# Performance work log

Measured on AMD Instinct MI355X. Metric: run time of the kernel, lower is better.

The kernel has to match this reference:

```python
import jax, jax.numpy as jnp
import numpy as np

# dims
B, T, C, D, H, NH, HD, INTER, L = 4, 1024, 256, 256, 512, 8, 64, 2048, 4
CF, CB, BASE = 0, 128, 10000.0  # context_forward, context_backward, rope theta


def _rope_tables():
    inv = 1.0 / (BASE ** (jnp.arange(0, HD, 2, dtype=jnp.float32) / HD))
    t = jnp.arange(T, dtype=jnp.float32)
    f = jnp.einsum('i,j->ij', t, inv)          # [T, HD/2]
    emb = jnp.concatenate([f, f], axis=-1)      # [T, HD]
    return jnp.cos(emb), jnp.sin(emb)


def _rotate_half(x):
    x1, x2 = jnp.split(x, 2, axis=-1)
    return jnp.concatenate([-x2, x1], axis=-1)


def _ln(x, g, b):
    m = x.mean(-1, keepdims=True)
    v = ((x - m) ** 2).mean(-1, keepdims=True)
    return (x - m) / jnp.sqrt(v + 1e-5) * g + b


def _band_mask():
    # create_context_mask(CF, CB, T): allow j in [i-CB, i+CF]
    i = jnp.arange(T)[:, None]
    j = jnp.arange(T)[None, :]
    return (j <= i + CF) & (j >= i - CB)  # [T, T] bool


def setup_inputs() -> dict:
    key = jax.random.key(0)
    ks = jax.random.split(key, 16)
    w = lambda k, shp: (0.02 * jax.random.normal(k, shp)).astype(jnp.float32)
    return {
        'spikes': jax.random.normal(ks[0], (B, T, C), dtype=jnp.float32),
        'spikes_mask': jnp.ones((B, T), dtype=jnp.int32),
        'spikes_timestamp': jnp.tile(jnp.arange(T, dtype=jnp.int32), (B, 1)),
        'embed_w': w(ks[1], (C, D)), 'embed_b': jnp.zeros((D,), jnp.float32),
        'proj_w': w(ks[2], (D, H)), 'proj_b': jnp.zeros((H,), jnp.float32),
        'ln1_g': jnp.ones((L, H), jnp.float32), 'ln1_b': jnp.zeros((L, H), jnp.float32),
        'Wq': w(ks[3], (L, H, H)), 'bq': jnp.zeros((L, H), jnp.float32),
        'Wk': w(ks[4], (L, H, H)), 'bk': jnp.zeros((L, H), jnp.float32),
        'Wv': w(ks[5], (L, H, H)), 'bv': jnp.zeros((L, H), jnp.float32),
        'Wo': w(ks[6], (L, H, H)), 'bo': jnp.zeros((L, H), jnp.float32),
        'ln2_g': jnp.ones((L, H), jnp.float32), 'ln2_b': jnp.zeros((L, H), jnp.float32),
        'up_w': w(ks[7], (L, H, INTER)), 'up_b': jnp.zeros((L, INTER), jnp.float32),
        'down_w': w(ks[8], (L, INTER, H)), 'down_b': jnp.zeros((L, H), jnp.float32),
    }


def reference(spikes, spikes_mask, spikes_timestamp, embed_w, embed_b, proj_w, proj_b,
              ln1_g, ln1_b, Wq, bq, Wk, bk, Wv, bv, Wo, bo, ln2_g, ln2_b,
              up_w, up_b, down_w, down_b):
    cos, sin = _rope_tables()
    mask = _band_mask()[None, None] & (spikes_mask[:, None, None, :] > 0)  # [B,1,T,T]
    cs = cos[spikes_timestamp][:, None]  # [B,1,T,HD]
    sn = sin[spikes_timestamp][:, None]
    neg = jnp.finfo(jnp.float32).min

    # NeuralEmbeddingLayer (no stack/pos/tokens): Linear -> gelu -> Linear
    x = jax.nn.gelu(spikes @ embed_w + embed_b, approximate=False) @ proj_w + proj_b

    for l in range(L):
        h = _ln(x, ln1_g[l], ln1_b[l])
        q = (h @ Wq[l] + bq[l]).reshape(B, T, NH, HD).transpose(0, 2, 1, 3)
        k = (h @ Wk[l] + bk[l]).reshape(B, T, NH, HD).transpose(0, 2, 1, 3)
        v = (h @ Wv[l] + bv[l]).reshape(B, T, NH, HD).transpose(0, 2, 1, 3)
        q = q * cs + _rotate_half(q) * sn
        k = k * cs + _rotate_half(k) * sn
        s = jnp.einsum('bhqd,bhkd->bhqk', q, k) / np.float32(np.sqrt(HD))
        s = jnp.where(mask, s, neg)
        p = jax.nn.softmax(s, axis=-1)
        o = jnp.einsum('bhqk,bhkd->bhqd', p, v).transpose(0, 2, 1, 3).reshape(B, T, H)
        x = x + o @ Wo[l] + bo[l]
        h = _ln(x, ln2_g[l], ln2_b[l])
        x = x + jax.nn.gelu(h @ up_w[l] + up_b[l], approximate=False) @ down_w[l] + down_b[l]
    return x
```

## Files before the change

### kernel.cpp

```cpp
#include <hip/hip_runtime.h>
#include <math.h>

#define B_ 4
#define T_ 1024
#define C_ 256
#define D_ 256
#define H_ 512
#define NH_ 8
#define HD_ 64
#define INTER_ 2048
#define L_ 4
#define CB_ 128

typedef short bf16x8 __attribute__((ext_vector_type(8)));
typedef unsigned short ush8 __attribute__((ext_vector_type(8)));
typedef float f32x4 __attribute__((ext_vector_type(4)));

__device__ __forceinline__ float gelu_exact(float x) {
    return 0.5f * x * (1.0f + erff(x * 0.70710678118654752f));
}

__device__ __forceinline__ unsigned short f2bf(float f) {
    unsigned u = __float_as_uint(f);
    u += 0x7fffu + ((u >> 16) & 1u);
    return (unsigned short)(u >> 16);
}
__device__ __forceinline__ float bf2f(unsigned short h) {
    return __uint_as_float((unsigned)h << 16);
}

__device__ __forceinline__ void xcd_swz(int& bx, int& by) {
    const int gx  = gridDim.x;
    const int nwg = gx * gridDim.y;
    int bid = blockIdx.y * gx + blockIdx.x;
    bid = (bid & 7) * (nwg >> 3) + (bid >> 3);
    bx = bid % gx;
    by = bid / gx;
}

template<int ACT, int RES, int OBF, int SPLIT>
__global__ __launch_bounds__(256) void mm64_k(
    const unsigned short* __restrict__ A, const unsigned short* __restrict__ BT,
    const float* __restrict__ b0, const float* __restrict__ b1,
    const float* __restrict__ b2,
    const float* res,
    void* o0, void* o1, void* o2,
    const int M, const int N, const int K)
{
    __shared__ unsigned short As[64 * 256];
    __shared__ unsigned short Bs[64 * 256];

    int bx, by; xcd_swz(bx, by);

    const int tid  = threadIdx.x;
    const int lane = tid & 63;
    const int w    = tid >> 6;
    const int m0   = by * 64;
    const int n0   = bx * 64;
    const int wm   = (w >> 1) * 32;
    const int wn   = (w & 1) * 32;
    const int l16  = lane & 15;
    const int g16  = lane >> 4;

    f32x4 acc[2][2] = {};

    const unsigned short* Abase = A  + (size_t)m0 * K;
    const unsigned short* Bbase = BT + (size_t)n0 * K;

    for (int k0 = 0; k0 < K; k0 += 256) {
        __syncthreads();
#pragma unroll
        for (int it = 0; it < 8; ++it) {
            const int c  = it * 256 + tid;
            const int rc = c >> 5;
            const int gk = (c & 31) ^ (rc & 7);
            __builtin_amdgcn_global_load_lds(
                (const __attribute__((address_space(1))) unsigned*)(Abase + (size_t)rc * K + k0 + gk * 8),
                (__attribute__((address_space(3))) unsigned*)(As + (size_t)(it * 256 + (w << 6)) * 8), 16, 0, 0);
        }
#pragma unroll
        for (int it = 0; it < 8; ++it) {
            const int c  = it * 256 + tid;
            const int rc = c >> 5;
            const int gk = (c & 31) ^ (rc & 7);
            __builtin_amdgcn_global_load_lds(
                (const __attribute__((address_space(1))) unsigned*)(Bbase + (size_t)rc * K + k0 + gk * 8),
                (__attribute__((address_space(3))) unsigned*)(Bs + (size_t)(it * 256 + (w << 6)) * 8), 16, 0, 0);
        }
        __syncthreads();

#pragma unroll
        for (int kk = 0; kk < 8; ++kk) {
            const int kf = kk * 4 + g16;
            const int sw = (kf ^ (l16 & 7)) * 8;
            bf16x8 a[2], b[2];
#pragma unroll
            for (int t = 0; t < 2; ++t)
                a[t] = *(const bf16x8*)&As[(wm + t * 16 + l16) * 256 + sw];
#pragma unroll
            for (int t = 0; t < 2; ++t)
                b[t] = *(const bf16x8*)&Bs[(wn + t * 16 + l16) * 256 + sw];
#pragma unroll
            for (int i = 0; i < 2; ++i)
#pragma unroll
                for (int j = 0; j < 2; ++j)
                    acc[i][j] = __builtin_amdgcn_mfma_f32_16x16x32_bf16(a[i], b[j], acc[i][j], 0, 0, 0);
        }
    }

    if (OBF || SPLIT) {
        __syncthreads();
        unsigned short* Eb = ((w < 2) ? As : Bs) + (w & 1) * 1024;
        const int row16 = lane >> 2;
        const int cg    = lane & 3;

        const int gnb   = n0 + wn;
        const int which = SPLIT ? (gnb >> 9) : 0;
        const int lnb   = SPLIT ? (gnb & 511) : gnb;
        const int ldo   = SPLIT ? 512 : N;
        unsigned short* oo = SPLIT
            ? ((which == 0) ? (unsigned short*)o0 : (which == 1) ? (unsigned short*)o1 : (unsigned short*)o2)
            : (unsigned short*)o0;
        const float* bb = SPLIT ? ((which == 0) ? b0 : (which == 1) ? b1 : b2) : b0;
        const float scale = (SPLIT && which == 0) ? 0.125f : 1.0f;

#pragma unroll
        for (int i = 0; i < 2; ++i) {
#pragma unroll
            for (int j = 0; j < 2; ++j) {
                const float bv = bb[lnb + j * 16 + l16];
#pragma unroll
                for (int r = 0; r < 4; ++r) {
                    float cv = acc[i][j][r] + bv;
                    if (ACT) cv = gelu_exact(cv);
                    if (SPLIT) cv *= scale;
                    Eb[(g16 * 4 + r) * 40 + j * 16 + l16] = f2bf(cv);
                }
            }
            const int grow0 = m0 + wm + i * 16 + row16;
#pragma unroll
            for (int s = 0; s < 2; ++s) {
                ushort4 t4 = *(const ushort4*)&Eb[row16 * 40 + s * 16 + cg * 4];
                *(ushort4*)&oo[(size_t)grow0 * ldo + lnb + s * 16 + cg * 4] = t4;
            }
        }
        return;
    }

#pragma unroll
    for (int i = 0; i < 2; ++i) {
        const int gmb = m0 + wm + i * 16 + g16 * 4;
#pragma unroll
        for (int j = 0; j < 2; ++j) {
            const int gn = n0 + wn + j * 16 + l16;
            const float bv = b0[gn];
#pragma unroll
            for (int r = 0; r < 4; ++r) {
                float cv = acc[i][j][r] + bv;
                if (ACT) cv = gelu_exact(cv);
                if (RES) cv += res[(size_t)(gmb + r) * 512 + gn];
                ((float*)o0)[(size_t)(gmb + r) * N + gn] = cv;
            }
        }
    }
}

template<int ACT, int RES, int OBF, int SPLIT, int BN>
__global__ __launch_bounds__(256) void mm128_k(
    const unsigned short* __restrict__ A, const unsigned short* __restrict__ BT,
    const float* __restrict__ b0, const float* __restrict__ b1,
    const float* __restrict__ b2,
    const float* res,
    void* o0, void* o1, void* o2,
    const int M, const int N, const int K)
{
    constexpr int NJ = BN / 32;

    __shared__ unsigned short As[128 * 128];
    __shared__ unsigned short Bs[BN * 128];

    int bx, by; xcd_swz(bx, by);

    const int tid  = threadIdx.x;
    const int lane = tid & 63;
    const int w    = tid >> 6;
    const int m0   = by * 128;
    const int n0   = bx * BN;
    const int wm   = (w >> 1) * 64;
    const int wn   = (w & 1) * (BN / 2);
    const int l16  = lane & 15;
    const int g16  = lane >> 4;

    f32x4 acc[4][NJ] = {};

    const unsigned short* Abase = A  + (size_t)m0 * K;
    const unsigned short* Bbase = BT + (size_t)n0 * K;

    for (int k0 = 0; k0 < K; k0 += 128) {
        __syncthreads();
#pragma unroll
        for (int it = 0; it < 8; ++it) {
            const int c  = it * 256 + tid;
            const int rc = c >> 4;
            const int gk = (c & 15) ^ (rc & 7);
            __builtin_amdgcn_global_load_lds(
                (const __attribute__((address_space(1))) unsigned*)(Abase + (size_t)rc * K + k0 + gk * 8),
                (__attribute__((address_space(3))) unsigned*)(As + (size_t)(it * 256 + (w << 6)) * 8), 16, 0, 0);
        }
#pragma unroll
        for (int it = 0; it < NJ * 2; ++it) {
            const int c  = it * 256 + tid;
            const int rc = c >> 4;
            const int gk = (c & 15) ^ (rc & 7);
            __builtin_amdgcn_global_load_lds(
                (const __attribute__((address_space(1))) unsigned*)(Bbase + (size_t)rc * K + k0 + gk * 8),
                (__attribute__((address_space(3))) unsigned*)(Bs + (size_t)(it * 256 + (w << 6)) * 8), 16, 0, 0);
        }
        __syncthreads();

#pragma unroll
        for (int kk = 0; kk < 4; ++kk) {
            const int kf = kk * 4 + g16;
            const int sw = (kf ^ (l16 & 7)) * 8;
            bf16x8 a[4], b[NJ];
#pragma unroll
            for (int t = 0; t < 4; ++t)
                a[t] = *(const bf16x8*)&As[(wm + t * 16 + l16) * 128 + sw];
#pragma unroll
            for (int t = 0; t < NJ; ++t)
                b[t] = *(const bf16x8*)&Bs[(wn + t * 16 + l16) * 128 + sw];
#pragma unroll
            for (int i = 0; i < 4; ++i)
#pragma unroll
                for (int j = 0; j < NJ; ++j)
                    acc[i][j] = __builtin_amdgcn_mfma_f32_16x16x32_bf16(a[i], b[j], acc[i][j], 0, 0, 0);
        }
    }

    if (OBF || SPLIT) {
        __syncthreads();
        constexpr int WC  = NJ * 16;
        constexpr int EST = WC + 8;
        constexpr int LPR = WC / 4;
        constexpr int RPI = 64 / LPR;
        unsigned short* Eb = As + w * (16 * EST);
        const int erow = lane / LPR;
        const int ecol = (lane % LPR) * 4;

        const int gnb   = n0 + wn;
        const int which = SPLIT ? (gnb >> 9) : 0;
        const int lnb   = SPLIT ? (gnb & 511) : gnb;
        const int ldo   = SPLIT ? 512 : N;
        unsigned short* oo = SPLIT
            ? ((which == 0) ? (unsigned short*)o0 : (which == 1) ? (unsigned short*)o1 : (unsigned short*)o2)
            : (unsigned short*)o0;
        const float* bb = SPLIT ? ((which == 0) ? b0 : (which == 1) ? b1 : b2) : b0;
        const float scale = (SPLIT && which == 0) ? 0.125f : 1.0f;

#pragma unroll
        for (int i = 0; i < 4; ++i) {
#pragma unroll
            for (int j = 0; j < NJ; ++j) {
                const float bv = bb[lnb + j * 16 + l16];
#pragma unroll
                for (int r = 0; r < 4; ++r) {
                    float cv = acc[i][j][r] + bv;
                    if (ACT) cv = gelu_exact(cv);
                    if (SPLIT) cv *= scale;
                    Eb[(g16 * 4 + r) * EST + j * 16 + l16] = f2bf(cv);
                }
            }
            const int grow0 = m0 + wm + i * 16;
#pragma unroll
            for (int s = 0; s < NJ; ++s) {
                ushort4 t4 = *(const ushort4*)&Eb[(s * RPI + erow) * EST + ecol];
                *(ushort4*)&oo[(size_t)(grow0 + s * RPI + erow) * ldo + lnb + ecol] = t4;
            }
        }
        return;
    }

#pragma unroll
    for (int i = 0; i < 4; ++i) {
        const int gmb = m0 + wm + i * 16 + g16 * 4;
#pragma unroll
        for (int j = 0; j < NJ; ++j) {
            const int gn = n0 + wn + j * 16 + l16;
            const float bv = b0[gn];
#pragma unroll
            for (int r = 0; r < 4; ++r) {
                float cv = acc[i][j][r] + bv;
                if (ACT) cv = gelu_exact(cv);
                if (RES) cv += res[(size_t)(gmb + r) * 512 + gn];
                ((float*)o0)[(size_t)(gmb + r) * N + gn] = cv;
            }
        }
    }
}

__global__ __launch_bounds__(256) void prep_k(
    const float* __restrict__ spikes,
    const float* __restrict__ embed_w, const float* __restrict__ proj_w,
    const float* __restrict__ Wq, const float* __restrict__ Wk,
    const float* __restrict__ Wv, const float* __restrict__ Wo,
    const float* __restrict__ up_w, const float* __restrict__ down_w,
    unsigned short* __restrict__ spbf,
    unsigned short* __restrict__ embT, unsigned short* __restrict__ projT,
    unsigned short* __restrict__ qkvT, unsigned short* __restrict__ woT,
    unsigned short* __restrict__ upT, unsigned short* __restrict__ downT)
{
    const int idx = blockIdx.x;
    const int tid = threadIdx.x;

    if (idx >= 3120) {
        const int base = (idx - 3120) * 4096 + tid * 16;
#pragma unroll
        for (int s = 0; s < 4; ++s) {
            float4 v = *(const float4*)&spikes[base + s * 4];
            ushort4 o = {f2bf(v.x), f2bf(v.y), f2bf(v.z), f2bf(v.w)};
            *(ushort4*)&spbf[base + s * 4] = o;
        }
        return;
    }

    const float* src; unsigned short* dst; int R, Cc, t;
    if (idx < 16)      { src = embed_w; dst = embT;  R = C_; Cc = D_; t = idx; }
    else if (idx < 48) { src = proj_w;  dst = projT; R = D_; Cc = H_; t = idx - 16; }
    else if (idx < 816) {
        const int j = idx - 48;
        const int wsel = j >> 8;
        const int l = (j & 255) >> 6;
        t = j & 63;
        src = ((wsel == 0) ? Wq : (wsel == 1) ? Wk : Wv) + (size_t)l * H_ * H_;
        dst = qkvT + (size_t)l * 3 * H_ * H_ + (size_t)wsel * H_ * H_;
        R = H_; Cc = H_;
    } else if (idx < 1072) {
        const int j = idx - 816; const int l = j >> 6; t = j & 63;
        src = Wo + (size_t)l * H_ * H_; dst = woT + (size_t)l * H_ * H_;
        R = H_; Cc = H_;
    } else if (idx < 2096) {
        const int j = idx - 1072; const int l = j >> 8; t = j & 255;
        src = up_w + (size_t)l * H_ * INTER_; dst = upT + (size_t)l * INTER_ * H_;
        R = H_; Cc = INTER_;
    } else {
        const int j = idx - 2096; const int l = j >> 8; t = j & 255;
        src = down_w + (size_t)l * INTER_ * H_; dst = downT + (size_t)l * H_ * INTER_;
        R = INTER_; Cc = H_;
    }
    const int ntx = Cc >> 6;
    const int c0 = (t % ntx) * 64, r0 = (t / ntx) * 64;

    __shared__ float tile[64][65];
    const int tr = tid >> 4, tc = (tid & 15) * 4;
#pragma unroll
    for (int i = 0; i < 4; ++i) {
        float4 v = *(const float4*)&src[(size_t)(r0 + tr + i * 16) * Cc + c0 + tc];
        tile[tr + i * 16][tc + 0] = v.x;
        tile[tr + i * 16][tc + 1] = v.y;
        tile[tr + i * 16][tc + 2] = v.z;
        tile[tr + i * 16][tc + 3] = v.w;
    }
    __syncthreads();
#pragma unroll
    for (int i = 0; i < 4; ++i) {
        const int n = tr + i * 16;
        ushort4 o;
        o.x = f2bf(tile[tc + 0][n]);
        o.y = f2bf(tile[tc + 1][n]);
        o.z = f2bf(tile[tc + 2][n]);
        o.w = f2bf(tile[tc + 3][n]);
        *(ushort4*)&dst[(size_t)(c0 + n) * R + r0 + tc] = o;
    }
}

__global__ __launch_bounds__(256) void ln_k(
    const float* __restrict__ x, const float* __restrict__ g,
    const float* __restrict__ b, unsigned short* __restrict__ out)
{
    const int row = blockIdx.x;
    const int tid = threadIdx.x;
    const float* xr = x + (size_t)row * H_;

    float v0 = xr[tid];
    float v1 = xr[tid + 256];

    float s = v0 + v1;
#pragma unroll
    for (int off = 32; off; off >>= 1) s += __shfl_xor(s, off);

    __shared__ float red[4];
    const int wave = tid >> 6;
    if ((tid & 63) == 0) red[wave] = s;
    __syncthreads();
    const float mean = (red[0] + red[1] + red[2] + red[3]) * (1.0f / (float)H_);

    const float d0 = v0 - mean, d1 = v1 - mean;
    float q = d0 * d0 + d1 * d1;
#pragma unroll
    for (int off = 32; off; off >>= 1) q += __shfl_xor(q, off);
    __syncthreads();
    if ((tid & 63) == 0) red[wave] = q;
    __syncthreads();
    const float var = (red[0] + red[1] + red[2] + red[3]) * (1.0f / (float)H_);
    const float rstd = rsqrtf(var + 1e-5f);

    out[(size_t)row * H_ + tid]       = f2bf(d0 * rstd * g[tid] + b[tid]);
    out[(size_t)row * H_ + tid + 256] = f2bf(d1 * rstd * g[tid + 256] + b[tid + 256]);
}

#define AWIN 192
#define AKS 72
#define AVS 200

__global__ __launch_bounds__(256) void attn_k(
    const unsigned short* __restrict__ q, const unsigned short* __restrict__ k,
    const unsigned short* __restrict__ v, const int* __restrict__ smask,
    const int* __restrict__ ts, unsigned short* __restrict__ o)
{
    __shared__ unsigned short Ks[AWIN * AKS];
    __shared__ unsigned short Vt[64 * AVS];
    unsigned short* const Pb = Ks;

    const int blk = blockIdx.x;
    const int qt = blk & 15;
    const int h  = (blk >> 4) & 7;
    const int b  = blk >> 7;
    const int tid  = threadIdx.x;
    const int lane = tid & 63;
    const int w    = tid >> 6;
    const int l16  = lane & 15;
    const int g16  = lane >> 4;

    const int qlo = qt * 64;
    const int klo = (qlo >= CB_) ? (qlo - CB_) : 0;
    const int tb  = b * 1024;

    bf16x8 qa0, qa1;
    {
        const int qrow = w * 16 + l16;
        const unsigned short* gq = q + ((size_t)(tb + qlo + qrow)) * 512 + h * 64;
        ush8 lo = *(const ush8*)&gq[g16 * 8];
        ush8 hi = *(const ush8*)&gq[g16 * 8 + 32];
        const float tstamp = (float)ts[tb + qlo + qrow];
#pragma unroll
        for (int j = 0; j < 8; ++j) {
            const int d = g16 * 8 + j;
            const float freq = __expf(-0.2878231366242558f * (float)d);
            const float ang = tstamp * freq;
            const float cc = __cosf(ang), ss = __sinf(ang);
            const float v1 = bf2f(lo[j]);
            const float v2 = bf2f(hi[j]);
            ((unsigned short*)&qa0)[j] = f2bf(v1 * cc - v2 * ss);
            ((unsigned short*)&qa1)[j] = f2bf(v2 * cc + v1 * ss);
        }
    }

    {
        const unsigned short* gk = k + ((size_t)(tb + klo)) * 512 + h * 64;
        for (int c = tid; c < AWIN * 8; c += 256) {
            const int row = c >> 3, c4 = (c & 7) * 4;
            ushort4 lo = *(const ushort4*)&gk[(size_t)row * 512 + c4];
            ushort4 hi = *(const ushort4*)&gk[(size_t)row * 512 + c4 + 32];
            const float tstamp = (float)ts[tb + klo + row];
            ushort4 olo, ohi;
#pragma unroll
            for (int j2 = 0; j2 < 4; ++j2) {
                const float freq = __expf(-0.2878231366242558f * (float)(c4 + j2));
                const float ang = tstamp * freq;
                const float cc = __cosf(ang), ss = __sinf(ang);
                const float v1 = bf2f(((const unsigned short*)&lo)[j2]);
                const float v2 = bf2f(((const unsigned short*)&hi)[j2]);
                ((unsigned short*)&olo)[j2] = f2bf(v1 * cc - v2 * ss);
                ((unsigned short*)&ohi)[j2] = f2bf(v2 * cc + v1 * ss);
            }
            *(ushort4*)&Ks[row * AKS + c4]      = olo;
            *(ushort4*)&Ks[row * AKS + c4 + 32] = ohi;
        }
    }
    {
        const unsigned short* gv = v + ((size_t)(tb + klo)) * 512 + h * 64;
        for (int c = tid; c < AWIN * 16; c += 256) {
            const int row = c >> 4, c4 = (c & 15) * 4;
            ushort4 vv = *(const ushort4*)&gv[(size_t)row * 512 + c4];
            Vt[(c4 + 0) * AVS + row] = vv.x;
            Vt[(c4 + 1) * AVS + row] = vv.y;
            Vt[(c4 + 2) * AVS + row] = vv.z;
            Vt[(c4 + 3) * AVS + row] = vv.w;
        }
    }
    __syncthreads();

    f32x4 accs[12];
#pragma unroll
    for (int t = 0; t < 12; ++t) {
        const bf16x8 b0 = *(const bf16x8*)&Ks[(t * 16 + l16) * AKS + g16 * 8];
        const bf16x8 b1 = *(const bf16x8*)&Ks[(t * 16 + l16) * AKS + 32 + g16 * 8];
        f32x4 c = {};
        c = __builtin_amdgcn_mfma_f32_16x16x32_bf16(qa0, b0, c, 0, 0, 0);
        c = __builtin_amdgcn_mfma_f32_16x16x32_bf16(qa1, b1, c, 0, 0, 0);
        accs[t] = c;
    }

    bool mk[12];
    int  jj[12];
#pragma unroll
    for (int t = 0; t < 12; ++t) {
        jj[t] = klo + t * 16 + l16;
        mk[t] = smask[tb + jj[t]] > 0;
    }

    float rs[4];
#pragma unroll
    for (int r = 0; r < 4; ++r) {
        const int i = qlo + 16 * w + g16 * 4 + r;
        float mx = -1e30f;
#pragma unroll
        for (int t = 0; t < 12; ++t) {
            const bool val = mk[t] && (jj[t] >= i - CB_) && (jj[t] <= i);
            mx = fmaxf(mx, val ? accs[t][r] : -1e30f);
        }
        mx = fmaxf(mx, __shfl_xor(mx, 1));
        mx = fmaxf(mx, __shfl_xor(mx, 2));
        mx = fmaxf(mx, __shfl_xor(mx, 4));
        mx = fmaxf(mx, __shfl_xor(mx, 8));
        float sum = 0.0f;
#pragma unroll
        for (int t = 0; t < 12; ++t) {
            const bool val = mk[t] && (jj[t] >= i - CB_) && (jj[t] <= i);
            const float p = val ? __expf(accs[t][r] - mx) : 0.0f;
            accs[t][r] = p;
            sum += p;
        }
        sum += __shfl_xor(sum, 1);
        sum += __shfl_xor(sum, 2);
        sum += __shfl_xor(sum, 4);
        sum += __shfl_xor(sum, 8);
        rs[r] = 1.0f / sum;
    }

    __syncthreads();

#pragma unroll
    for (int t = 0; t < 12; ++t)
#pragma unroll
        for (int r = 0; r < 4; ++r)
            Pb[(16 * w + g16 * 4 + r) * AVS + t * 16 + l16] = f2bf(accs[t][r]);

    f32x4 acco[4];
#pragma unroll
    for (int nt = 0; nt < 4; ++nt) {
        f32x4 c = {};
#pragma unroll
        for (int ks = 0; ks < 6; ++ks) {
            const bf16x8 a = *(const bf16x8*)&Pb[(16 * w + l16) * AVS + ks * 32 + g16 * 8];
            const bf16x8 bb = *(const bf16x8*)&Vt[(nt * 16 + l16) * AVS + ks * 32 + g16 * 8];
            c = __builtin_amdgcn_mfma_f32_16x16x32_bf16(a, bb, c, 0, 0, 0);
        }
        acco[nt] = c;
    }

    __syncthreads();
#pragma unroll
    for (int nt = 0; nt < 4; ++nt)
#pragma unroll
        for (int r = 0; r < 4; ++r)
            Pb[(16 * w + g16 * 4 + r) * AVS + nt * 16 + l16] = f2bf(acco[nt][r] * rs[r]);

    const int row16 = lane >> 2, cg = lane & 3;
    const int grow = tb + qlo + 16 * w + row16;
#pragma unroll
    for (int s = 0; s < 4; ++s) {
        ushort4 t4 = *(const ushort4*)&Pb[(16 * w + row16) * AVS + s * 16 + cg * 4];
        *(ushort4*)&o[(size_t)grow * 512 + h * 64 + s * 16 + cg * 4] = t4;
    }
}

extern "C" void kernel_launch(void* const* d_in, const int* in_sizes, int n_in,
                              void* d_out, int out_size, void* d_ws, size_t ws_size,
                              hipStream_t stream)
{
    const float* spikes  = (const float*)d_in[0];
    const int*   smask   = (const int*)d_in[1];
    const int*   ts      = (const int*)d_in[2];
    const float* embed_w = (const float*)d_in[3];
    const float* embed_b = (const float*)d_in[4];
    const float* proj_w  = (const float*)d_in[5];
    const float* proj_b  = (const float*)d_in[6];
    const float* ln1_g   = (const float*)d_in[7];
    const float* ln1_b   = (const float*)d_in[8];
    const float* Wq      = (const float*)d_in[9];
    const float* bq      = (const float*)d_in[10];
    const float* Wk      = (const float*)d_in[11];
    const float* bk      = (const float*)d_in[12];
    const float* Wv      = (const float*)d_in[13];
    const float* bv      = (const float*)d_in[14];
    const float* Wo      = (const float*)d_in[15];
    const float* bo      = (const float*)d_in[16];
    const float* ln2_g   = (const float*)d_in[17];
    const float* ln2_b   = (const float*)d_in[18];
    const float* up_w    = (const float*)d_in[19];
    const float* up_b    = (const float*)d_in[20];
    const float* down_w  = (const float*)d_in[21];
    const float* down_b  = (const float*)d_in[22];

    const int M = B_ * T_;

    char* p = (char*)d_ws;
    float* x = (float*)p;                       p += (size_t)M * H_ * 4;
    unsigned short* qb  = (unsigned short*)p;   p += (size_t)M * H_ * 2;
    unsigned short* kb  = (unsigned short*)p;   p += (size_t)M * H_ * 2;
    unsigned short* vb  = (unsigned short*)p;   p += (size_t)M * H_ * 2;
    unsigned short* hbf = (unsigned short*)p;   p += (size_t)M * H_ * 2;
    unsigned short* obf = (unsigned short*)p;   p += (size_t)M * H_ * 2;
    unsigned short* ibf = (unsigned short*)p;   p += (size_t)M * INTER_ * 2;
    unsigned short* tbf = (unsigned short*)p;   p += (size_t)M * D_ * 2;
    unsigned short* spbf  = (unsigned short*)p; p += (size_t)M * C_ * 2;
    unsigned short* embT  = (unsigned short*)p; p += (size_t)D_ * C_ * 2;
    unsigned short* projT = (unsigned short*)p; p += (size_t)H_ * D_ * 2;
    unsigned short* qkvT  = (unsigned short*)p; p += (size_t)L_ * 3 * H_ * H_ * 2;
    unsigned short* woT   = (unsigned short*)p; p += (size_t)L_ * H_ * H_ * 2;
    unsigned short* upT   = (unsigned short*)p; p += (size_t)L_ * INTER_ * H_ * 2;
    unsigned short* downT = (unsigned short*)p; p += (size_t)L_ * H_ * INTER_ * 2;

    prep_k<<<3376, 256, 0, stream>>>(
        spikes, embed_w, proj_w, Wq, Wk, Wv, Wo, up_w, down_w,
        spbf, embT, projT, qkvT, woT, upT, downT);

    mm64_k<1, 0, 1, 0><<<dim3(D_ / 64, M / 64), 256, 0, stream>>>(
        spbf, embT, embed_b, nullptr, nullptr, nullptr,
        tbf, nullptr, nullptr, M, D_, C_);
    mm64_k<0, 0, 0, 0><<<dim3(H_ / 64, M / 64), 256, 0, stream>>>(
        tbf, projT, proj_b, nullptr, nullptr, nullptr,
        x, nullptr, nullptr, M, H_, D_);

    for (int l = 0; l < L_; ++l) {
        const unsigned short* qkvT_l = qkvT + (size_t)l * 3 * H_ * H_;
        const unsigned short* woT_l  = woT  + (size_t)l * H_ * H_;
        const unsigned short* upT_l  = upT  + (size_t)l * INTER_ * H_;
        const unsigned short* dnT_l  = downT + (size_t)l * H_ * INTER_;

        ln_k<<<M, 256, 0, stream>>>(x, ln1_g + l * H_, ln1_b + l * H_, hbf);

        mm128_k<0, 0, 1, 1, 64><<<dim3((3 * H_) / 64, M / 128), 256, 0, stream>>>(
            hbf, qkvT_l, bq + l * H_, bk + l * H_, bv + l * H_, nullptr,
            qb, kb, vb, M, 3 * H_, H_);

        attn_k<<<B_ * NH_ * (T_ / 64), 256, 0, stream>>>(qb, kb, vb, smask, ts, obf);

        mm64_k<0, 1, 0, 0><<<dim3(H_ / 64, M / 64), 256, 0, stream>>>(
            obf, woT_l, bo + l * H_, nullptr, nullptr, x,
            x, nullptr, nullptr, M, H_, H_);

        ln_k<<<M, 256, 0, stream>>>(x, ln2_g + l * H_, ln2_b + l * H_, hbf);

        mm128_k<1, 0, 1, 0, 128><<<dim3(INTER_ / 128, M / 128), 256, 0, stream>>>(
            hbf, upT_l, up_b + l * INTER_, nullptr, nullptr, nullptr,
            ibf, nullptr, nullptr, M, INTER_, H_);

        float* dst = (l == L_ - 1) ? (float*)d_out : x;
        mm64_k<0, 1, 0, 0><<<dim3(H_ / 64, M / 64), 256, 0, stream>>>(
            ibf, dnT_l, down_b + l * H_, nullptr, nullptr, x,
            dst, nullptr, nullptr, M, H_, INTER_);
    }
}
```

Baseline: 493.8 us.

## Precompute RoPE cos/sin table once and make LayerNorm one row per wave

Adds a RoPE cos/sin table, computed once per call in extra prep_k blocks from the timestamps, and has the attention kernel read it instead of evaluating exp/cos/sin for every Q and K element in every layer. LayerNorm now gives each row to one wavefront with vectorized float4 loads and shuffle-only reductions, which removes the shared-memory reductions and block barriers and cuts the block count by four. In exchange the table adds global-memory traffic (M*32 float2 values) and the prep kernel launches extra blocks.

```diff
diff --git a/kernel.cpp b/kernel.cpp
--- a/kernel.cpp
+++ b/kernel.cpp
@@ -304,13 +304,29 @@
     const float* __restrict__ Wq, const float* __restrict__ Wk,
     const float* __restrict__ Wv, const float* __restrict__ Wo,
     const float* __restrict__ up_w, const float* __restrict__ down_w,
+    const int* __restrict__ ts,
     unsigned short* __restrict__ spbf,
     unsigned short* __restrict__ embT, unsigned short* __restrict__ projT,
     unsigned short* __restrict__ qkvT, unsigned short* __restrict__ woT,
-    unsigned short* __restrict__ upT, unsigned short* __restrict__ downT)
+    unsigned short* __restrict__ upT, unsigned short* __restrict__ downT,
+    float2* __restrict__ rope_tab)
 {
     const int idx = blockIdx.x;
     const int tid = threadIdx.x;
+
+    if (idx >= 3376) {
+        const int e0 = (idx - 3376) * 4096 + tid * 16;
+#pragma unroll
+        for (int i = 0; i < 16; ++i) {
+            const int e = e0 + i;
+            const int row = e >> 5, d = e & 31;
+            const float tstamp = (float)ts[row];
+            const float freq = __expf(-0.2878231366242558f * (float)d);
+            const float ang = tstamp * freq;
+            rope_tab[e] = make_float2(__cosf(ang), __sinf(ang));
+        }
+        return;
+    }
 
     if (idx >= 3120) {
         const int base = (idx - 3120) * 4096 + tid * 16;
@@ -377,35 +393,46 @@
     const float* __restrict__ x, const float* __restrict__ g,
     const float* __restrict__ b, unsigned short* __restrict__ out)
 {
-    const int row = blockIdx.x;
-    const int tid = threadIdx.x;
+    const int wave = threadIdx.x >> 6;
+    const int lane = threadIdx.x & 63;
+    const int row  = blockIdx.x * 4 + wave;
     const float* xr = x + (size_t)row * H_;
-
-    float v0 = xr[tid];
-    float v1 = xr[tid + 256];
-
-    float s = v0 + v1;
+    const int c0 = lane * 8;
+
+    float4 a0 = *(const float4*)&xr[c0];
+    float4 a1 = *(const float4*)&xr[c0 + 4];
+
+    float s = a0.x + a0.y + a0.z + a0.w + a1.x + a1.y + a1.z + a1.w;
 #pragma unroll
     for (int off = 32; off; off >>= 1) s += __shfl_xor(s, off);
-
-    __shared__ float red[4];
-    const int wave = tid >> 6;
-    if ((tid & 63) == 0) red[wave] = s;
-    __syncthreads();
-    const float mean = (red[0] + red[1] + red[2] + red[3]) * (1.0f / (float)H_);
-
-    const float d0 = v0 - mean, d1 = v1 - mean;
-    float q = d0 * d0 + d1 * d1;
+    const float mean = s * (1.0f / (float)H_);
+
+    float d[8];
+    d[0] = a0.x - mean; d[1] = a0.y - mean; d[2] = a0.z - mean; d[3] = a0.w - mean;
+    d[4] = a1.x - mean; d[5] = a1.y - mean; d[6] = a1.z - mean; d[7] = a1.w - mean;
+    float q = 0.0f;
+#pragma unroll
+    for (int j = 0; j < 8; ++j) q += d[j] * d[j];
 #pragma unroll
     for (int off = 32; off; off >>= 1) q += __shfl_xor(q, off);
-    __syncthreads();
-    if ((tid & 63) == 0) red[wave] = q;
-    __syncthreads();
-    const float var = (red[0] + red[1] + red[2] + red[3]) * (1.0f / (float)H_);
-    const float rstd = rsqrtf(var + 1e-5f);
-
-    out[(size_t)row * H_ + tid]       = f2bf(d0 * rstd * g[tid] + b[tid]);
-    out[(size_t)row * H_ + tid + 256] = f2bf(d1 * rstd * g[tid + 256] + b[tid + 256]);
+    const float rstd = rsqrtf(q * (1.0f / (float)H_) + 1e-5f);
+
+    float4 g0 = *(const float4*)&g[c0];
+    float4 g1 = *(const float4*)&g[c0 + 4];
+    float4 b0 = *(const float4*)&b[c0];
+    float4 b1 = *(const float4*)&b[c0 + 4];
+
+    ushort4 o0, o1;
+    o0.x = f2bf(d[0] * rstd * g0.x + b0.x);
+    o0.y = f2bf(d[1] * rstd * g0.y + b0.y);
+    o0.z = f2bf(d[2] * rstd * g0.z + b0.z);
+    o0.w = f2bf(d[3] * rstd * g0.w + b0.w);
+    o1.x = f2bf(d[4] * rstd * g1.x + b1.x);
+    o1.y = f2bf(d[5] * rstd * g1.y + b1.y);
+    o1.z = f2bf(d[6] * rstd * g1.z + b1.z);
+    o1.w = f2bf(d[7] * rstd * g1.w + b1.w);
+    *(ushort4*)&out[(size_t)row * H_ + c0]     = o0;
+    *(ushort4*)&out[(size_t)row * H_ + c0 + 4] = o1;
 }
 
 #define AWIN 192
@@ -415,7 +442,7 @@
 __global__ __launch_bounds__(256) void attn_k(
     const unsigned short* __restrict__ q, const unsigned short* __restrict__ k,
     const unsigned short* __restrict__ v, const int* __restrict__ smask,
-    const int* __restrict__ ts, unsigned short* __restrict__ o)
+    const float2* __restrict__ rope_tab, unsigned short* __restrict__ o)
 {
     __shared__ unsigned short Ks[AWIN * AKS];
     __shared__ unsigned short Vt[64 * AVS];
@@ -441,17 +468,14 @@
         const unsigned short* gq = q + ((size_t)(tb + qlo + qrow)) * 512 + h * 64;
         ush8 lo = *(const ush8*)&gq[g16 * 8];
         ush8 hi = *(const ush8*)&gq[g16 * 8 + 32];
-        const float tstamp = (float)ts[tb + qlo + qrow];
+        const float2* tr = rope_tab + (size_t)(tb + qlo + qrow) * 32 + g16 * 8;
 #pragma unroll
         for (int j = 0; j < 8; ++j) {
-            const int d = g16 * 8 + j;
-            const float freq = __expf(-0.2878231366242558f * (float)d);
-            const float ang = tstamp * freq;
-            const float cc = __cosf(ang), ss = __sinf(ang);
+            const float2 cs = tr[j];
             const float v1 = bf2f(lo[j]);
             const float v2 = bf2f(hi[j]);
-            ((unsigned short*)&qa0)[j] = f2bf(v1 * cc - v2 * ss);
-            ((unsigned short*)&qa1)[j] = f2bf(v2 * cc + v1 * ss);
+            ((unsigned short*)&qa0)[j] = f2bf(v1 * cs.x - v2 * cs.y);
+            ((unsigned short*)&qa1)[j] = f2bf(v2 * cs.x + v1 * cs.y);
         }
     }
 
@@ -461,17 +485,15 @@
             const int row = c >> 3, c4 = (c & 7) * 4;
             ushort4 lo = *(const ushort4*)&gk[(size_t)row * 512 + c4];
             ushort4 hi = *(const ushort4*)&gk[(size_t)row * 512 + c4 + 32];
-            const float tstamp = (float)ts[tb + klo + row];
+            const float2* tr = rope_tab + (size_t)(tb + klo + row) * 32 + c4;
             ushort4 olo, ohi;
 #pragma unroll
             for (int j2 = 0; j2 < 4; ++j2) {
-                const float freq = __expf(-0.2878231366242558f * (float)(c4 + j2));
-                const float ang = tstamp * freq;
-                const float cc = __cosf(ang), ss = __sinf(ang);
+                const float2 cs = tr[j2];
                 const float v1 = bf2f(((const unsigned short*)&lo)[j2]);
                 const float v2 = bf2f(((const unsigned short*)&hi)[j2]);
-                ((unsigned short*)&olo)[j2] = f2bf(v1 * cc - v2 * ss);
-                ((unsigned short*)&ohi)[j2] = f2bf(v2 * cc + v1 * ss);
+                ((unsigned short*)&olo)[j2] = f2bf(v1 * cs.x - v2 * cs.y);
+                ((unsigned short*)&ohi)[j2] = f2bf(v2 * cs.x + v1 * cs.y);
             }
             *(ushort4*)&Ks[row * AKS + c4]      = olo;
             *(ushort4*)&Ks[row * AKS + c4 + 32] = ohi;
@@ -621,10 +643,11 @@
     unsigned short* woT   = (unsigned short*)p; p += (size_t)L_ * H_ * H_ * 2;
     unsigned short* upT   = (unsigned short*)p; p += (size_t)L_ * INTER_ * H_ * 2;
     unsigned short* downT = (unsigned short*)p; p += (size_t)L_ * H_ * INTER_ * 2;
-
-    prep_k<<<3376, 256, 0, stream>>>(
-        spikes, embed_w, proj_w, Wq, Wk, Wv, Wo, up_w, down_w,
-        spbf, embT, projT, qkvT, woT, upT, downT);
+    float2* rope_tab = (float2*)p;              p += (size_t)M * 32 * sizeof(float2);
+
+    prep_k<<<3408, 256, 0, stream>>>(
+        spikes, embed_w, proj_w, Wq, Wk, Wv, Wo, up_w, down_w, ts,
+        spbf, embT, projT, qkvT, woT, upT, downT, rope_tab);
 
     mm64_k<1, 0, 1, 0><<<dim3(D_ / 64, M / 64), 256, 0, stream>>>(
         spbf, embT, embed_b, nullptr, nullptr, nullptr,
@@ -639,19 +662,20 @@
         const unsigned short* upT_l  = upT  + (size_t)l * INTER_ * H_;
         const unsigned short* dnT_l  = downT + (size_t)l * H_ * INTER_;
 
-        ln_k<<<M, 256, 0, stream>>>(x, ln1_g + l * H_, ln1_b + l * H_, hbf);
+        ln_k<<<M / 4, 256, 0, stream>>>(x, ln1_g + l * H_, ln1_b + l * H_, hbf);
 
         mm128_k<0, 0, 1, 1, 64><<<dim3((3 * H_) / 64, M / 128), 256, 0, stream>>>(
             hbf, qkvT_l, bq + l * H_, bk + l * H_, bv + l * H_, nullptr,
             qb, kb, vb, M, 3 * H_, H_);
 
-        attn_k<<<B_ * NH_ * (T_ / 64), 256, 0, stream>>>(qb, kb, vb, smask, ts, obf);
+        attn_k<<<B_ * NH_ * (T_ / 64), 256, 0, stream>>>(qb, kb, vb, smask,
+                                                         rope_tab, obf);
 
         mm64_k<0, 1, 0, 0><<<dim3(H_ / 64, M / 64), 256, 0, stream>>>(
             obf, woT_l, bo + l * H_, nullptr, nullptr, x,
             x, nullptr, nullptr, M, H_, H_);
 
-        ln_k<<<M, 256, 0, stream>>>(x, ln2_g + l * H_, ln2_b + l * H_, hbf);
+        ln_k<<<M / 4, 256, 0, stream>>>(x, ln2_g + l * H_, ln2_b + l * H_, hbf);
 
         mm128_k<1, 0, 1, 0, 128><<<dim3(INTER_ / 128, M / 128), 256, 0, stream>>>(
             hbf, upT_l, up_b + l * INTER_, nullptr, nullptr, nullptr,
```

Measured after the change: 483.5 us, median of 4. -2.1%, faster.
